# Optimization experiments

Measured on AMD Instinct MI355X. Metric: run time of the kernel, lower is better.

## Reference

```python
import jax, jax.numpy as jnp
import numpy as np

N_NODES = 50000
ALPHA_SLOPE = 0.2  # LeakyReLU negative slope
EPS = 1e-16


def setup_inputs() -> dict:
    key = jax.random.key(0)
    k1, k2, k3, k4 = jax.random.split(key, 4)
    in_features, heads, d = 512, 8, 32
    x = jax.random.normal(k1, (N_NODES, in_features), dtype=jnp.float32)
    edge_index = jax.random.randint(k2, (2, 800000), 0, N_NODES, dtype=jnp.int64)
    # xavier_normal with relu gain ~ sqrt(2) * sqrt(2/(fan_in+fan_out))
    w_std = np.sqrt(2.0) * np.sqrt(2.0 / (in_features + d))
    a_std = np.sqrt(2.0) * np.sqrt(2.0 / (1 + 2 * d))
    W = jax.random.normal(k3, (heads, in_features, d), dtype=jnp.float32) * w_std
    a = jax.random.normal(k4, (heads, 2 * d), dtype=jnp.float32) * a_std
    return {"x": x, "edge_index": edge_index, "W": W, "a": a}


def reference(x, edge_index, W, a):
    # x: [N, F_in], edge_index: [2, E], W: [H, F_in, D], a: [H, 2D]
    n = x.shape[0]
    d = W.shape[-1]
    e0, e1 = edge_index[0], edge_index[1]
    # per-head projected features: [N, H, D]
    h = jnp.einsum('nf,hfd->nhd', x, W)
    # attention logits: a.mm(cat(h[e0], h[e1]).T) == a_src.h[e0] + a_dst.h[e1]
    a_src, a_dst = a[:, :d], a[:, d:]          # [H, D] each
    s_src = jnp.einsum('nhd,hd->nh', h, a_src)  # [N, H]
    s_dst = jnp.einsum('nhd,hd->nh', h, a_dst)  # [N, H]
    logits = s_src[e0] + s_dst[e1]              # [E, H]
    logits = jnp.where(logits >= 0, logits, ALPHA_SLOPE * logits)  # LeakyReLU
    # segment softmax over destination node e0
    m = jax.ops.segment_max(logits, e0, num_segments=n)   # [N, H]
    ex = jnp.exp(logits - m[e0])                          # [E, H]
    denom = jax.ops.segment_sum(ex, e0, num_segments=n)   # [N, H]
    alpha = ex / (denom[e0] + EPS)                        # [E, H]
    # dropout is identity in eval mode
    # sparse aggregate: out[e0] += alpha * h[e1]
    msg = alpha[:, :, None] * h[e1]                       # [E, H, D]
    out = jax.ops.segment_sum(msg, e0, num_segments=n)    # [N, H, D]
    return out.reshape(n, -1)                             # concat heads -> [N, H*D]
```

## Files before the change

kernel.cpp:

```cpp
#include <hip/hip_runtime.h>

#define N_NODES 50000
#define N_EDGES 800000
#define IN_F    512
#define HEADS   8
#define DHEAD   32
#define NHD     256
#define SLOPE   0.2f
#define EPS_F   1e-16f
#define N_SBLK  ((N_NODES + 255) / 256)
#define NB_GEMM ((N_NODES + 63) / 64)
#define NB_HIST ((N_EDGES + 4095) / 4096)

typedef __attribute__((ext_vector_type(8))) short short8;
typedef __attribute__((ext_vector_type(4))) float f32x4;
typedef __attribute__((ext_vector_type(4))) unsigned short u16x4;

__device__ __forceinline__ unsigned short f2bf(float f) {
  unsigned int u = __float_as_uint(f);
  unsigned int r = u + 0x7FFFu + ((u >> 16) & 1u);
  return (unsigned short)(r >> 16);
}
__device__ __forceinline__ float bf2f(unsigned short s) {
  return __uint_as_float(((unsigned int)s) << 16);
}
__device__ __forceinline__ void gload_lds16(const void* g, void* l) {
  __builtin_amdgcn_global_load_lds((const __attribute__((address_space(1))) void*)g,
                                   (__attribute__((address_space(3))) void*)l, 16, 0, 0);
}

__global__ void k_cast_w(const float* __restrict__ W, unsigned short* __restrict__ WbT,
                         int* __restrict__ deg) {
  int id = blockIdx.x * blockDim.x + threadIdx.x;
  if (id < NHD * IN_F) {
    int c = id >> 9, k = id & 511;
    WbT[id] = f2bf(W[(c >> 5) * (IN_F * DHEAD) + k * DHEAD + (c & 31)]);
  }
  if (id < N_NODES) deg[id] = 0;
}

__global__ __launch_bounds__(256) void k_gemm_mfma(const float* __restrict__ x,
                                                   const unsigned short* __restrict__ WbT,
                                                   unsigned short* __restrict__ hb,
                                                   const float* __restrict__ a,
                                                   float* __restrict__ s_src,
                                                   float* __restrict__ s_dst,
                                                   const int* __restrict__ ei,
                                                   int* __restrict__ deg) {
  if (blockIdx.x >= NB_GEMM) {
    int b = blockIdx.x - NB_GEMM;
    int end = min(b * 4096 + 4096, N_EDGES);
    for (int e = b * 4096 + threadIdx.x; e < end; e += 256)
      atomicAdd(&deg[ei[e]], 1);
    return;
  }

  __shared__ unsigned short As[64 * 64];
  __shared__ unsigned short Bs[256 * 64];
  const int tid  = threadIdx.x;
  const int lane = tid & 63;
  const int wid  = tid >> 6;
  const int bm   = blockIdx.x * 64;
  const int wn   = wid * 64;

  const int arow = tid >> 3, ap = tid & 7, aq = ap ^ (arow & 7);
  const float* gA0 = x + (size_t)min(bm + arow,      N_NODES - 1) * IN_F + aq * 8;
  const float* gA1 = x + (size_t)min(bm + arow + 32, N_NODES - 1) * IN_F + aq * 8;
  unsigned short* lA0 = &As[(arow * 8 + ap) * 8];
  unsigned short* lA1 = &As[((arow + 32) * 8 + ap) * 8];

  const int bs = 512 * wid + lane;
  const int brow = bs >> 3, bp = bs & 7, bq = bp ^ (brow & 7);
  const unsigned short* gB = WbT + (size_t)brow * IN_F + bq * 8;
  unsigned short* lB = &Bs[(size_t)512 * wid * 8];

  f32x4 acc[4][4] = {};

  for (int k0 = 0; k0 < IN_F; k0 += 64) {
    __syncthreads();
#pragma unroll
    for (int it = 0; it < 8; ++it)
      gload_lds16(gB + k0 + it * 8 * IN_F, lB + it * 64 * 8);
    {
      float4 a00 = *(const float4*)(gA0 + k0);
      float4 a01 = *(const float4*)(gA0 + k0 + 4);
      float4 a10 = *(const float4*)(gA1 + k0);
      float4 a11 = *(const float4*)(gA1 + k0 + 4);
      short8 v0, v1;
      v0[0] = (short)f2bf(a00.x); v0[1] = (short)f2bf(a00.y);
      v0[2] = (short)f2bf(a00.z); v0[3] = (short)f2bf(a00.w);
      v0[4] = (short)f2bf(a01.x); v0[5] = (short)f2bf(a01.y);
      v0[6] = (short)f2bf(a01.z); v0[7] = (short)f2bf(a01.w);
      v1[0] = (short)f2bf(a10.x); v1[1] = (short)f2bf(a10.y);
      v1[2] = (short)f2bf(a10.z); v1[3] = (short)f2bf(a10.w);
      v1[4] = (short)f2bf(a11.x); v1[5] = (short)f2bf(a11.y);
      v1[6] = (short)f2bf(a11.z); v1[7] = (short)f2bf(a11.w);
      *(short8*)lA0 = v0;
      *(short8*)lA1 = v1;
    }
    __syncthreads();

#pragma unroll
    for (int kk = 0; kk < 2; ++kk) {
      short8 af[4], bfr[4];
#pragma unroll
      for (int i = 0; i < 4; ++i) {
        int r = i * 16 + (lane & 15);
        int q = kk * 4 + (lane >> 4);
        af[i] = *(const short8*)&As[(r * 8 + (q ^ (r & 7))) * 8];
      }
#pragma unroll
      for (int j = 0; j < 4; ++j) {
        int r = wn + j * 16 + (lane & 15);
        int q = kk * 4 + (lane >> 4);
        bfr[j] = *(const short8*)&Bs[(r * 8 + (q ^ (r & 7))) * 8];
      }
#pragma unroll
      for (int i = 0; i < 4; ++i)
#pragma unroll
        for (int j = 0; j < 4; ++j)
          acc[i][j] = __builtin_amdgcn_mfma_f32_16x16x32_bf16(af[i], bfr[j], acc[i][j], 0, 0, 0);
    }
  }

  const int h0 = 2 * wid, h1 = 2 * wid + 1;
  const int dl = lane & 15;
  const float as00 = a[h0 * 64 + dl],      as01 = a[h0 * 64 + 16 + dl];
  const float as10 = a[h1 * 64 + dl],      as11 = a[h1 * 64 + 16 + dl];
  const float ad00 = a[h0 * 64 + 32 + dl], ad01 = a[h0 * 64 + 48 + dl];
  const float ad10 = a[h1 * 64 + 32 + dl], ad11 = a[h1 * 64 + 48 + dl];

#pragma unroll
  for (int i = 0; i < 4; ++i) {
#pragma unroll
    for (int q = 0; q < 4; ++q) {
      int row = bm + i * 16 + (lane >> 4) * 4 + q;
      float ss0 = acc[i][0][q] * as00 + acc[i][1][q] * as01;
      float ss1 = acc[i][2][q] * as10 + acc[i][3][q] * as11;
      float sd0 = acc[i][0][q] * ad00 + acc[i][1][q] * ad01;
      float sd1 = acc[i][2][q] * ad10 + acc[i][3][q] * ad11;
#pragma unroll
      for (int o = 1; o < 16; o <<= 1) {
        ss0 += __shfl_xor(ss0, o);
        ss1 += __shfl_xor(ss1, o);
        sd0 += __shfl_xor(sd0, o);
        sd1 += __shfl_xor(sd1, o);
      }
      if (row < N_NODES) {
#pragma unroll
        for (int j = 0; j < 4; ++j)
          hb[(size_t)row * NHD + wn + j * 16 + dl] = f2bf(acc[i][j][q]);
        if (dl == 0) {
          s_src[row * 8 + h0] = ss0;
          s_src[row * 8 + h1] = ss1;
          s_dst[row * 8 + h0] = sd0;
          s_dst[row * 8 + h1] = sd1;
        }
      }
    }
  }
}

__global__ __launch_bounds__(256) void k_bsum(const int* __restrict__ deg,
                                              int* __restrict__ bsum) {
  __shared__ int sm[4];
  int i = blockIdx.x * 256 + threadIdx.x;
  int v = (i < N_NODES) ? deg[i] : 0;
#pragma unroll
  for (int o = 1; o < 64; o <<= 1) v += __shfl_xor(v, o);
  if ((threadIdx.x & 63) == 0) sm[threadIdx.x >> 6] = v;
  __syncthreads();
  if (threadIdx.x == 0) bsum[blockIdx.x] = sm[0] + sm[1] + sm[2] + sm[3];
}

__global__ __launch_bounds__(256) void k_scan_main(const int* __restrict__ deg,
                                                   const int* __restrict__ bsum,
                                                   int* __restrict__ rowptr,
                                                   int* __restrict__ cursor) {
  __shared__ int sb[256];
  __shared__ int sm[256];
  const int t = threadIdx.x;
  const int b = blockIdx.x;
  int bv = (t < N_SBLK) ? bsum[t] : 0;
  sb[t] = bv;
  int i = b * 256 + t;
  int v = (i < N_NODES) ? deg[i] : 0;
  sm[t] = v;
  __syncthreads();
#pragma unroll
  for (int o = 1; o < 256; o <<= 1) {
    int u1 = (t >= o) ? sb[t - o] : 0;
    int u2 = (t >= o) ? sm[t - o] : 0;
    __syncthreads();
    sb[t] += u1;
    sm[t] += u2;
    __syncthreads();
  }
  int boff = (b > 0) ? sb[b - 1] : 0;
  if (i < N_NODES) {
    int ex = boff + sm[t] - v;
    rowptr[i] = ex;
    cursor[i] = ex;
  }
  if (b == 0 && t == 0) rowptr[N_NODES] = sb[255];
}

__global__ void k_fill(const int* __restrict__ ei, int* __restrict__ cursor,
                       int* __restrict__ edst) {
  int e = blockIdx.x * blockDim.x + threadIdx.x;
  if (e >= N_EDGES) return;
  int p = atomicAdd(&cursor[ei[e]], 1);
  edst[p] = ei[N_EDGES + e];
}

__global__ __launch_bounds__(256) void k_aggr(const int* __restrict__ rowptr,
                                              const int* __restrict__ edst,
                                              const float* __restrict__ s_src,
                                              const float* __restrict__ s_dst,
                                              const unsigned short* __restrict__ hb,
                                              float* __restrict__ out) {
  int n = (int)((blockIdx.x * blockDim.x + threadIdx.x) >> 6);
  if (n >= N_NODES) return;
  n = __builtin_amdgcn_readfirstlane(n);
  const int lane = threadIdx.x & 63;
  const int head = lane >> 3;
  const float ssrc = s_src[n * 8 + head];
  int i = rowptr[n];
  const int iend = rowptr[n + 1];
  float den = 0.f;
  f32x4 acc = {0.f, 0.f, 0.f, 0.f};
  for (; i + 1 < iend; i += 2) {
    int d0 = edst[i], d1 = edst[i + 1];
    float v0 = ssrc + s_dst[d0 * 8 + head];
    float v1 = ssrc + s_dst[d1 * 8 + head];
    u16x4 h0 = *(const u16x4*)(hb + (size_t)d0 * NHD + lane * 4);
    u16x4 h1 = *(const u16x4*)(hb + (size_t)d1 * NHD + lane * 4);
    v0 = v0 >= 0.f ? v0 : SLOPE * v0;
    v1 = v1 >= 0.f ? v1 : SLOPE * v1;
    float e0 = __expf(v0), e1 = __expf(v1);
    den += e0 + e1;
    acc.x += e0 * bf2f(h0.x) + e1 * bf2f(h1.x);
    acc.y += e0 * bf2f(h0.y) + e1 * bf2f(h1.y);
    acc.z += e0 * bf2f(h0.z) + e1 * bf2f(h1.z);
    acc.w += e0 * bf2f(h0.w) + e1 * bf2f(h1.w);
  }
  if (i < iend) {
    int d0 = edst[i];
    float v0 = ssrc + s_dst[d0 * 8 + head];
    v0 = v0 >= 0.f ? v0 : SLOPE * v0;
    float e0 = __expf(v0);
    u16x4 h0 = *(const u16x4*)(hb + (size_t)d0 * NHD + lane * 4);
    den += e0;
    acc.x += e0 * bf2f(h0.x);
    acc.y += e0 * bf2f(h0.y);
    acc.z += e0 * bf2f(h0.z);
    acc.w += e0 * bf2f(h0.w);
  }
  float inv = 1.f / (den + EPS_F);
  *(f32x4*)(out + (size_t)n * NHD + lane * 4) = acc * inv;
}

extern "C" void kernel_launch(void* const* d_in, const int* in_sizes, int n_in,
                              void* d_out, int out_size, void* d_ws, size_t ws_size,
                              hipStream_t stream) {
  const float* x  = (const float*)d_in[0];
  const int*   ei = (const int*)d_in[1];
  const float* W  = (const float*)d_in[2];
  const float* a  = (const float*)d_in[3];
  float* out = (float*)d_out;

  unsigned short* hb  = (unsigned short*)d_ws;
  unsigned short* WbT = hb + (size_t)N_NODES * NHD;
  float* s_src = (float*)(WbT + (size_t)NHD * IN_F);
  float* s_dst = s_src + (size_t)N_NODES * HEADS;
  int* deg    = (int*)(s_dst + (size_t)N_NODES * HEADS);
  int* cursor = deg + N_NODES;
  int* rowptr = cursor + N_NODES;
  int* bsum   = rowptr + 50008;
  int* edst   = bsum + 256;

  k_cast_w<<<512, 256, 0, stream>>>(W, WbT, deg);
  k_gemm_mfma<<<NB_GEMM + NB_HIST, 256, 0, stream>>>(x, WbT, hb, a, s_src, s_dst, ei, deg);
  k_bsum<<<N_SBLK, 256, 0, stream>>>(deg, bsum);
  k_scan_main<<<N_SBLK, 256, 0, stream>>>(deg, bsum, rowptr, cursor);
  k_fill<<<(N_EDGES + 255) / 256, 256, 0, stream>>>(ei, cursor, edst);
  k_aggr<<<(N_NODES * 64 + 255) / 256, 256, 0, stream>>>(rowptr, edst, s_src, s_dst, hb, out);
}
```

Measured before the change: 192.0 us.

## Pre-swizzle W into MFMA fragment order and drop LDS staging in projection GEMM

The weight cast kernel now writes W in bf16 already arranged in the exact per-lane MFMA B-fragment order. The GEMM then loads B fragments straight from global memory with coalesced 16-byte loads and reads and converts x fragments directly per lane, so it no longer uses shared memory or __syncthreads. Warps are regrouped into a 2x2 layout covering 32 rows by 128 columns each. This removes LDS traffic and barriers, but each warp now fetches its own B data and x rows from global or L2, so there is more redundant global traffic and more register pressure.

```diff
diff --git a/kernel.cpp b/kernel.cpp
--- a/kernel.cpp
+++ b/kernel.cpp
@@ -24,18 +24,21 @@
 __device__ __forceinline__ float bf2f(unsigned short s) {
   return __uint_as_float(((unsigned int)s) << 16);
 }
-__device__ __forceinline__ void gload_lds16(const void* g, void* l) {
-  __builtin_amdgcn_global_load_lds((const __attribute__((address_space(1))) void*)g,
-                                   (__attribute__((address_space(3))) void*)l, 16, 0, 0);
-}
-
-__global__ void k_cast_w(const float* __restrict__ W, unsigned short* __restrict__ WbT,
-                         int* __restrict__ deg) {
-  int id = blockIdx.x * blockDim.x + threadIdx.x;
-  if (id < NHD * IN_F) {
-    int c = id >> 9, k = id & 511;
-    WbT[id] = f2bf(W[(c >> 5) * (IN_F * DHEAD) + k * DHEAD + (c & 31)]);
-  }
+
+__global__ __launch_bounds__(256) void k_cast_w(const float* __restrict__ W,
+                                                unsigned short* __restrict__ WbT,
+                                                int* __restrict__ deg) {
+  int id = blockIdx.x * 256 + threadIdx.x;
+  int chunk = id >> 3, e = id & 7;
+  int lane = chunk & 63;
+  int t = chunk >> 6;
+  int j = t & 7;  t >>= 3;
+  int wn2 = t & 1; t >>= 1;
+  int kk = t & 1;  t >>= 1;
+  int k0s = t;
+  int c = wn2 * 128 + j * 16 + (lane & 15);
+  int k = k0s * 64 + (kk * 4 + (lane >> 4)) * 8 + e;
+  WbT[id] = f2bf(W[(c >> 5) * (IN_F * DHEAD) + k * DHEAD + (c & 31)]);
   if (id < N_NODES) deg[id] = 0;
 }
 
@@ -55,106 +58,90 @@
     return;
   }
 
-  __shared__ unsigned short As[64 * 64];
-  __shared__ unsigned short Bs[256 * 64];
   const int tid  = threadIdx.x;
   const int lane = tid & 63;
   const int wid  = tid >> 6;
+  const int wm   = wid >> 1;
+  const int wn2  = wid & 1;
   const int bm   = blockIdx.x * 64;
-  const int wn   = wid * 64;
-
-  const int arow = tid >> 3, ap = tid & 7, aq = ap ^ (arow & 7);
-  const float* gA0 = x + (size_t)min(bm + arow,      N_NODES - 1) * IN_F + aq * 8;
-  const float* gA1 = x + (size_t)min(bm + arow + 32, N_NODES - 1) * IN_F + aq * 8;
-  unsigned short* lA0 = &As[(arow * 8 + ap) * 8];
-  unsigned short* lA1 = &As[((arow + 32) * 8 + ap) * 8];
-
-  const int bs = 512 * wid + lane;
-  const int brow = bs >> 3, bp = bs & 7, bq = bp ^ (brow & 7);
-  const unsigned short* gB = WbT + (size_t)brow * IN_F + bq * 8;
-  unsigned short* lB = &Bs[(size_t)512 * wid * 8];
-
-  f32x4 acc[4][4] = {};
-
-  for (int k0 = 0; k0 < IN_F; k0 += 64) {
-    __syncthreads();
-#pragma unroll
-    for (int it = 0; it < 8; ++it)
-      gload_lds16(gB + k0 + it * 8 * IN_F, lB + it * 64 * 8);
-    {
-      float4 a00 = *(const float4*)(gA0 + k0);
-      float4 a01 = *(const float4*)(gA0 + k0 + 4);
-      float4 a10 = *(const float4*)(gA1 + k0);
-      float4 a11 = *(const float4*)(gA1 + k0 + 4);
-      short8 v0, v1;
-      v0[0] = (short)f2bf(a00.x); v0[1] = (short)f2bf(a00.y);
-      v0[2] = (short)f2bf(a00.z); v0[3] = (short)f2bf(a00.w);
-      v0[4] = (short)f2bf(a01.x); v0[5] = (short)f2bf(a01.y);
-      v0[6] = (short)f2bf(a01.z); v0[7] = (short)f2bf(a01.w);
-      v1[0] = (short)f2bf(a10.x); v1[1] = (short)f2bf(a10.y);
-      v1[2] = (short)f2bf(a10.z); v1[3] = (short)f2bf(a10.w);
-      v1[4] = (short)f2bf(a11.x); v1[5] = (short)f2bf(a11.y);
-      v1[6] = (short)f2bf(a11.z); v1[7] = (short)f2bf(a11.w);
-      *(short8*)lA0 = v0;
-      *(short8*)lA1 = v1;
-    }
-    __syncthreads();
-
+  const int dl   = lane & 15;
+  const int qg   = lane >> 4;
+
+  const float* xr[2];
+#pragma unroll
+  for (int i = 0; i < 2; ++i)
+    xr[i] = x + (size_t)min(bm + wm * 32 + i * 16 + dl, N_NODES - 1) * IN_F + qg * 8;
+
+  f32x4 acc[2][8] = {};
+
+#pragma unroll 2
+  for (int k0s = 0; k0s < 8; ++k0s) {
 #pragma unroll
     for (int kk = 0; kk < 2; ++kk) {
-      short8 af[4], bfr[4];
-#pragma unroll
-      for (int i = 0; i < 4; ++i) {
-        int r = i * 16 + (lane & 15);
-        int q = kk * 4 + (lane >> 4);
-        af[i] = *(const short8*)&As[(r * 8 + (q ^ (r & 7))) * 8];
-      }
-#pragma unroll
-      for (int j = 0; j < 4; ++j) {
-        int r = wn + j * 16 + (lane & 15);
-        int q = kk * 4 + (lane >> 4);
-        bfr[j] = *(const short8*)&Bs[(r * 8 + (q ^ (r & 7))) * 8];
-      }
-#pragma unroll
-      for (int i = 0; i < 4; ++i)
-#pragma unroll
-        for (int j = 0; j < 4; ++j)
+      const unsigned short* bp =
+          WbT + (((size_t)((k0s * 2 + kk) * 2 + wn2) * 8) * 64 + lane) * 8;
+      short8 bfr[8];
+#pragma unroll
+      for (int j = 0; j < 8; ++j) bfr[j] = *(const short8*)(bp + (size_t)j * 64 * 8);
+      short8 af[2];
+#pragma unroll
+      for (int i = 0; i < 2; ++i) {
+        const float* ap = xr[i] + k0s * 64 + kk * 32;
+        float4 lo = *(const float4*)ap;
+        float4 hi = *(const float4*)(ap + 4);
+        short8 v;
+        v[0] = (short)f2bf(lo.x); v[1] = (short)f2bf(lo.y);
+        v[2] = (short)f2bf(lo.z); v[3] = (short)f2bf(lo.w);
+        v[4] = (short)f2bf(hi.x); v[5] = (short)f2bf(hi.y);
+        v[6] = (short)f2bf(hi.z); v[7] = (short)f2bf(hi.w);
+        af[i] = v;
+      }
+#pragma unroll
+      for (int i = 0; i < 2; ++i)
+#pragma unroll
+        for (int j = 0; j < 8; ++j)
           acc[i][j] = __builtin_amdgcn_mfma_f32_16x16x32_bf16(af[i], bfr[j], acc[i][j], 0, 0, 0);
     }
   }
 
-  const int h0 = 2 * wid, h1 = 2 * wid + 1;
-  const int dl = lane & 15;
-  const float as00 = a[h0 * 64 + dl],      as01 = a[h0 * 64 + 16 + dl];
-  const float as10 = a[h1 * 64 + dl],      as11 = a[h1 * 64 + 16 + dl];
-  const float ad00 = a[h0 * 64 + 32 + dl], ad01 = a[h0 * 64 + 48 + dl];
-  const float ad10 = a[h1 * 64 + 32 + dl], ad11 = a[h1 * 64 + 48 + dl];
-
-#pragma unroll
-  for (int i = 0; i < 4; ++i) {
+  float as_[8], ad_[8];
+#pragma unroll
+  for (int j = 0; j < 8; ++j) {
+    int hh = wn2 * 4 + (j >> 1);
+    int d  = (j & 1) * 16 + dl;
+    as_[j] = a[hh * 64 + d];
+    ad_[j] = a[hh * 64 + 32 + d];
+  }
+#pragma unroll
+  for (int i = 0; i < 2; ++i) {
 #pragma unroll
     for (int q = 0; q < 4; ++q) {
-      int row = bm + i * 16 + (lane >> 4) * 4 + q;
-      float ss0 = acc[i][0][q] * as00 + acc[i][1][q] * as01;
-      float ss1 = acc[i][2][q] * as10 + acc[i][3][q] * as11;
-      float sd0 = acc[i][0][q] * ad00 + acc[i][1][q] * ad01;
-      float sd1 = acc[i][2][q] * ad10 + acc[i][3][q] * ad11;
+      int row = bm + wm * 32 + i * 16 + qg * 4 + q;
+      float ss[4] = {0.f, 0.f, 0.f, 0.f};
+      float sd[4] = {0.f, 0.f, 0.f, 0.f};
+#pragma unroll
+      for (int j = 0; j < 8; ++j) {
+        ss[j >> 1] += acc[i][j][q] * as_[j];
+        sd[j >> 1] += acc[i][j][q] * ad_[j];
+      }
 #pragma unroll
       for (int o = 1; o < 16; o <<= 1) {
-        ss0 += __shfl_xor(ss0, o);
-        ss1 += __shfl_xor(ss1, o);
-        sd0 += __shfl_xor(sd0, o);
-        sd1 += __shfl_xor(sd1, o);
+#pragma unroll
+        for (int h2 = 0; h2 < 4; ++h2) {
+          ss[h2] += __shfl_xor(ss[h2], o);
+          sd[h2] += __shfl_xor(sd[h2], o);
+        }
       }
       if (row < N_NODES) {
 #pragma unroll
-        for (int j = 0; j < 4; ++j)
-          hb[(size_t)row * NHD + wn + j * 16 + dl] = f2bf(acc[i][j][q]);
+        for (int j = 0; j < 8; ++j)
+          hb[(size_t)row * NHD + wn2 * 128 + j * 16 + dl] = f2bf(acc[i][j][q]);
         if (dl == 0) {
-          s_src[row * 8 + h0] = ss0;
-          s_src[row * 8 + h1] = ss1;
-          s_dst[row * 8 + h0] = sd0;
-          s_dst[row * 8 + h1] = sd1;
+#pragma unroll
+          for (int h2 = 0; h2 < 4; ++h2) {
+            s_src[row * 8 + wn2 * 4 + h2] = ss[h2];
+            s_dst[row * 8 + wn2 * 4 + h2] = sd[h2];
+          }
         }
       }
     }
```

Measured after the change: 194.2 us. About the same (+1.2%).
